# Optimization experiments

Measured on AMD Instinct MI355X. Metric: run time of the kernel, lower is better.

The kernel has to match this reference:

```python
import jax, jax.numpy as jnp
import numpy as np

EMBED_DIM = 1024
NUM_HEADS = 16
HEAD_DIM = EMBED_DIM // NUM_HEADS
B, S = 2, 2048


def setup_inputs() -> dict:
    key = jax.random.key(0)
    ks = jax.random.split(key, 11)
    scale = 1.0 / np.sqrt(EMBED_DIM)
    inp = {
        "q": jax.random.normal(ks[0], (B, S, EMBED_DIM), jnp.float32),
        "k": jax.random.normal(ks[1], (B, S, EMBED_DIM), jnp.float32),
        "v": jax.random.normal(ks[2], (B, S, EMBED_DIM), jnp.float32),
        "Wq": jax.random.normal(ks[3], (EMBED_DIM, EMBED_DIM), jnp.float32) * scale,
        "bq": jnp.zeros((EMBED_DIM,), jnp.float32),
        "Wk": jax.random.normal(ks[4], (EMBED_DIM, EMBED_DIM), jnp.float32) * scale,
        "bk": jnp.zeros((EMBED_DIM,), jnp.float32),
        "Wv": jax.random.normal(ks[5], (EMBED_DIM, EMBED_DIM), jnp.float32) * scale,
        "bv": jnp.zeros((EMBED_DIM,), jnp.float32),
        "Wo": jax.random.normal(ks[6], (EMBED_DIM, EMBED_DIM), jnp.float32) * scale,
        "bo": jnp.zeros((EMBED_DIM,), jnp.float32),
    }
    return inp


def _split_heads(x):
    # [B, S, E] -> [B, H, S, D]
    b, s, _ = x.shape
    return x.reshape(b, s, NUM_HEADS, HEAD_DIM).transpose(0, 2, 1, 3)


def reference(q, k, v, Wq, bq, Wk, bk, Wv, bv, Wo, bo):
    query = _split_heads(q @ Wq + bq)  # [B,H,S,D]
    key_ = _split_heads(k @ Wk + bk)
    value = _split_heads(v @ Wv + bv)
    # scaled dot-product attention (scale by sqrt(head_dim), as in source)
    logits = jnp.einsum("bhqd,bhkd->bhqk", query, key_) / jnp.sqrt(
        jnp.asarray(HEAD_DIM, jnp.float32)
    )
    weights = jax.nn.softmax(logits, axis=-1)
    attn = jnp.einsum("bhqk,bhkd->bhqd", weights, value)  # [B,H,S,D]
    concat = attn.transpose(0, 2, 1, 3).reshape(q.shape[0], -1, EMBED_DIM)
    return concat @ Wo + bo
```

## Files before the change

kernel.cpp:

```cpp
#include <hip/hip_runtime.h>
#include <hip/hip_bf16.h>
#include <math.h>


typedef short bf16x8 __attribute__((ext_vector_type(8)));
typedef short bf16x4 __attribute__((ext_vector_type(4)));
typedef float f32x4 __attribute__((ext_vector_type(4)));
typedef unsigned short u16;
typedef unsigned int u32;

#if defined(__HIP_DEVICE_COMPILE__) && __has_builtin(__builtin_amdgcn_mfma_f32_16x16x16_bf16)
#define MFMA16(a, b, c) __builtin_amdgcn_mfma_f32_16x16x16_bf16(a, b, c, 0, 0, 0)
#else
#define MFMA16(a, b, c) __builtin_amdgcn_mfma_f32_16x16x16bf16_1k(a, b, c, 0, 0, 0)
#endif

#define QSCALE 0.18033688011112042f

__device__ __forceinline__ u16 f2b(float f) {
  union { float f; unsigned u; } v; v.f = f;
  unsigned r = v.u + 0x7FFF + ((v.u >> 16) & 1);
  return (u16)(r >> 16);
}

__device__ __forceinline__ void glds16(const u16* g, u16* l) {
  __builtin_amdgcn_global_load_lds(
      (const __attribute__((address_space(1))) u32*)g,
      (__attribute__((address_space(3))) u32*)l, 16, 0, 0);
}

__global__ void cvt3_f32_bf16(const float* __restrict__ q, const float* __restrict__ k,
                              const float* __restrict__ v, u16* __restrict__ qo,
                              u16* __restrict__ ko, u16* __restrict__ vo) {
  const float* in = blockIdx.y == 0 ? q : (blockIdx.y == 1 ? k : v);
  u16* out = blockIdx.y == 0 ? qo : (blockIdx.y == 1 ? ko : vo);
  int i = (blockIdx.x * 256 + threadIdx.x) * 8;
  float4 a = *(const float4*)(in + i);
  float4 b = *(const float4*)(in + i + 4);
  union { u16 u[8]; uint4 v; } o;
  o.u[0] = f2b(a.x); o.u[1] = f2b(a.y); o.u[2] = f2b(a.z); o.u[3] = f2b(a.w);
  o.u[4] = f2b(b.x); o.u[5] = f2b(b.y); o.u[6] = f2b(b.z); o.u[7] = f2b(b.w);
  *(uint4*)(out + i) = o.v;
}

__global__ void transpose_w4(const float* __restrict__ W0, const float* __restrict__ W1,
                             const float* __restrict__ W2, const float* __restrict__ W3,
                             u16* __restrict__ T0, u16* __restrict__ T1,
                             u16* __restrict__ T2, u16* __restrict__ T3) {
  const float* W = blockIdx.z == 0 ? W0 : (blockIdx.z == 1 ? W1 : (blockIdx.z == 2 ? W2 : W3));
  u16* WT = blockIdx.z == 0 ? T0 : (blockIdx.z == 1 ? T1 : (blockIdx.z == 2 ? T2 : T3));
  __shared__ float tile[64][65];
  int k0 = blockIdx.y * 64, n0 = blockIdx.x * 64;
  int c = threadIdx.x & 63, r0 = threadIdx.x >> 6;
  #pragma unroll
  for (int i = 0; i < 64; i += 4)
    tile[r0 + i][c] = W[(k0 + r0 + i) * 1024 + n0 + c];
  __syncthreads();
  #pragma unroll
  for (int i = 0; i < 64; i += 4)
    WT[(n0 + r0 + i) * 1024 + k0 + c] = f2b(tile[c][r0 + i]);
}

template<int MODE>
__device__ __forceinline__ void gemm_core(
    const u16* __restrict__ A, const u16* __restrict__ BT,
    const float* __restrict__ bias, void* __restrict__ out,
    int bx, int by, float scale) {
  __shared__ u16 As[128 * 64];
  __shared__ u16 Bs[128 * 64];
  const int tid = threadIdx.x;
  const int w = tid >> 6, lane = tid & 63;
  const int wm = w >> 1, wn = w & 1;
  const int q = lane >> 4, l16 = lane & 15;
  const int m0 = by * 128, n0 = bx * 128;
  const int K = 1024;

  f32x4 acc[4][4] = {};
  for (int k0 = 0; k0 < K; k0 += 64) {
    __syncthreads();
    #pragma unroll
    for (int p = 0; p < 4; ++p) {
      int c = p * 4 + w;
      int ci = c * 64 + lane;
      int r = ci >> 3, b = ci & 7;
      glds16(A + (m0 + r) * K + k0 + ((b ^ (r & 7)) * 8), As + c * 512);
    }
    #pragma unroll
    for (int p = 0; p < 4; ++p) {
      int c = p * 4 + w;
      int ci = c * 64 + lane;
      int r = ci >> 3, b = ci & 7;
      glds16(BT + (n0 + r) * K + k0 + ((b ^ (r & 7)) * 8), Bs + c * 512);
    }
    __builtin_amdgcn_s_waitcnt(0xF70);
    __syncthreads();
    #pragma unroll
    for (int ks = 0; ks < 2; ++ks) {
      bf16x8 af[4], bf[4];
      #pragma unroll
      for (int mt = 0; mt < 4; ++mt) {
        int row = wm * 64 + mt * 16 + l16;
        af[mt] = *(const bf16x8*)(As + row * 64 + (((ks * 4 + q) ^ (row & 7)) * 8));
      }
      #pragma unroll
      for (int nt = 0; nt < 4; ++nt) {
        int row = wn * 64 + nt * 16 + l16;
        bf[nt] = *(const bf16x8*)(Bs + row * 64 + (((ks * 4 + q) ^ (row & 7)) * 8));
      }
      #pragma unroll
      for (int mt = 0; mt < 4; ++mt)
        #pragma unroll
        for (int nt = 0; nt < 4; ++nt)
          acc[mt][nt] = __builtin_amdgcn_mfma_f32_16x16x32_bf16(af[mt], bf[nt], acc[mt][nt], 0, 0, 0);
    }
  }
  #pragma unroll
  for (int mt = 0; mt < 4; ++mt)
    #pragma unroll
    for (int nt = 0; nt < 4; ++nt) {
      int col = n0 + wn * 64 + nt * 16 + l16;
      float bcol = bias[col];
      if (MODE == 2) {
        int rbase = m0 + wm * 64 + mt * 16 + q * 4;
        int b = rbase >> 11, s0 = rbase & 2047;
        int h = col >> 6, d = col & 63;
        union { u16 u[4]; uint2 v; } o;
        #pragma unroll
        for (int reg = 0; reg < 4; ++reg)
          o.u[reg] = f2b(acc[mt][nt][reg] + bcol);
        *(uint2*)((u16*)out + (((b << 4) + h) * 64 + d) * 2048 + s0) = o.v;
      } else {
        #pragma unroll
        for (int reg = 0; reg < 4; ++reg) {
          int row = m0 + wm * 64 + mt * 16 + q * 4 + reg;
          float val = (acc[mt][nt][reg] + bcol) * scale;
          if (MODE == 0) {
            int b = row >> 11, s = row & 2047, h = col >> 6, d = col & 63;
            ((u16*)out)[(((b << 4) + h) * 2048 + s) * 64 + d] = f2b(val);
          } else {
            ((float*)out)[row * 1024 + col] = val;
          }
        }
      }
    }
}

__global__ __launch_bounds__(256) void gemm_qkv(
    const u16* qb, const u16* kb, const u16* vb,
    const u16* WqT, const u16* WkT, const u16* WvT,
    const float* bq, const float* bk, const float* bv,
    u16* Qh, u16* Kh, u16* VhT) {
  int z = blockIdx.z;
  if (z == 0)      gemm_core<0>(qb, WqT, bq, Qh,  blockIdx.x, blockIdx.y, QSCALE);
  else if (z == 1) gemm_core<0>(kb, WkT, bk, Kh,  blockIdx.x, blockIdx.y, 1.0f);
  else             gemm_core<2>(vb, WvT, bv, VhT, blockIdx.x, blockIdx.y, 1.0f);
}

__global__ __launch_bounds__(256) void gemm_out(
    const u16* A, const u16* BT, const float* bias, float* out) {
  gemm_core<1>(A, BT, bias, out, blockIdx.x, blockIdx.y, 1.0f);
}

__global__ __launch_bounds__(256) void flash_attn(
    const u16* __restrict__ Qh, const u16* __restrict__ Kh,
    const u16* __restrict__ VTh, u16* __restrict__ Oo) {
  __shared__ u16 Ks[2][64 * 64];
  __shared__ u16 Vt[2][64 * 64];

  const int tid = threadIdx.x, w = tid >> 6, lane = tid & 63;
  const int q = lane >> 4, l16 = lane & 15;
  const int bh = blockIdx.x >> 4, qt = blockIdx.x & 15;
  const u16* Qp = Qh + (bh * 2048 + qt * 128) * 64;
  const u16* Kp = Kh + bh * 2048 * 64;
  const u16* Vp = VTh + bh * 64 * 2048;

  bf16x8 aq[2][2];
  #pragma unroll
  for (int rb = 0; rb < 2; ++rb)
    #pragma unroll
    for (int ks = 0; ks < 2; ++ks)
      aq[rb][ks] = *(const bf16x8*)(Qp + (w * 32 + rb * 16 + l16) * 64 + ks * 32 + q * 8);

  const int sr = (lane & 7) ^ (lane >> 3);
  auto stage = [&](int kt2, int buf) {
    #pragma unroll
    for (int p = 0; p < 2; ++p) {
      int c = p * 4 + w;
      int r = c * 8 + (lane >> 3);
      glds16(Kp + (kt2 * 64 + r) * 64 + sr * 8, &Ks[buf][c * 512]);
      glds16(Vp + r * 2048 + kt2 * 64 + sr * 8, &Vt[buf][c * 512]);
    }
  };
  stage(0, 0);

  f32x4 oacc[4][2] = {};
  float lacc[2] = {0.f, 0.f};

  for (int kt = 0; kt < 32; ++kt) {
    const int cur = kt & 1;
    __builtin_amdgcn_s_waitcnt(0xF70);
    __syncthreads();
    if (kt + 1 < 32) stage(kt + 1, cur ^ 1);

    f32x4 st[2][4] = {};
    #pragma unroll
    for (int ks = 0; ks < 2; ++ks) {
      bf16x8 bk[4];
      #pragma unroll
      for (int nt = 0; nt < 4; ++nt) {
        int row = nt * 16 + l16;
        bk[nt] = *(const bf16x8*)(&Ks[cur][row * 64 + (((ks * 4 + q) ^ (l16 & 7)) * 8)]);
      }
      #pragma unroll
      for (int rb = 0; rb < 2; ++rb)
        #pragma unroll
        for (int nt = 0; nt < 4; ++nt)
          st[rb][nt] = __builtin_amdgcn_mfma_f32_16x16x32_bf16(bk[nt], aq[rb][ks], st[rb][nt], 0, 0, 0);
    }

    #pragma unroll
    for (int rb = 0; rb < 2; ++rb)
      #pragma unroll
      for (int nt = 0; nt < 4; ++nt)
        #pragma unroll
        for (int reg = 0; reg < 4; ++reg) {
          float p = __builtin_amdgcn_exp2f(st[rb][nt][reg]);
          lacc[rb] += p;
          st[rb][nt][reg] = p;
        }

    #pragma unroll
    for (int kb = 0; kb < 4; ++kb) {
      bf16x4 pf[2];
      #pragma unroll
      for (int rb = 0; rb < 2; ++rb) {
        union { u32 u[2]; bf16x4 v; } pk;
        pk.u[0] = __builtin_amdgcn_perm(__float_as_uint(st[rb][kb][1]),
                                        __float_as_uint(st[rb][kb][0]), 0x07060302u);
        pk.u[1] = __builtin_amdgcn_perm(__float_as_uint(st[rb][kb][3]),
                                        __float_as_uint(st[rb][kb][2]), 0x07060302u);
        pf[rb] = pk.v;
      }
      #pragma unroll
      for (int ntd = 0; ntd < 4; ++ntd) {
        int row = ntd * 16 + l16;
        int c = kb * 2 + (q >> 1);
        bf16x4 vf = *(const bf16x4*)(&Vt[cur][row * 64 + ((c ^ (l16 & 7)) * 8) + (q & 1) * 4]);
        #pragma unroll
        for (int rb = 0; rb < 2; ++rb)
          oacc[ntd][rb] = MFMA16(vf, pf[rb], oacc[ntd][rb]);
      }
    }
  }

  float rl[2];
  #pragma unroll
  for (int rb = 0; rb < 2; ++rb) {
    float s = lacc[rb];
    s += __shfl_xor(s, 16);
    s += __shfl_xor(s, 32);
    rl[rb] = 0.998046875f / s;
  }

  const int b = bh >> 4, h = bh & 15;
  #pragma unroll
  for (int rb = 0; rb < 2; ++rb) {
    int row = b * 2048 + qt * 128 + w * 32 + rb * 16 + l16;
    #pragma unroll
    for (int ntd = 0; ntd < 4; ++ntd) {
      union { u16 u[4]; uint2 v; } o;
      #pragma unroll
      for (int reg = 0; reg < 4; ++reg)
        o.u[reg] = f2b(oacc[ntd][rb][reg] * rl[rb]);
      *(uint2*)(Oo + row * 1024 + h * 64 + ntd * 16 + q * 4) = o.v;
    }
  }
}

extern "C" void kernel_launch(void* const* d_in, const int* in_sizes, int n_in,
                              void* d_out, int out_size, void* d_ws, size_t ws_size,
                              hipStream_t stream) {
  const float* q  = (const float*)d_in[0];
  const float* k  = (const float*)d_in[1];
  const float* v  = (const float*)d_in[2];
  const float* Wq = (const float*)d_in[3];
  const float* bq = (const float*)d_in[4];
  const float* Wk = (const float*)d_in[5];
  const float* bk = (const float*)d_in[6];
  const float* Wv = (const float*)d_in[7];
  const float* bv = (const float*)d_in[8];
  const float* Wo = (const float*)d_in[9];
  const float* bo = (const float*)d_in[10];

  char* ws = (char*)d_ws;
  const size_t MB = 1024 * 1024;
  u16* qb  = (u16*)(ws);
  u16* kb  = (u16*)(ws + 8 * MB);
  u16* vb  = (u16*)(ws + 16 * MB);
  u16* WqT = (u16*)(ws + 24 * MB);
  u16* WkT = (u16*)(ws + 26 * MB);
  u16* WvT = (u16*)(ws + 28 * MB);
  u16* WoT = (u16*)(ws + 30 * MB);
  u16* Qh  = (u16*)(ws + 32 * MB);
  u16* Kh  = (u16*)(ws + 40 * MB);
  u16* VhT = (u16*)(ws + 48 * MB);
  u16* Ao  = (u16*)(ws + 56 * MB);

  cvt3_f32_bf16<<<dim3(2048, 3), 256, 0, stream>>>(q, k, v, qb, kb, vb);
  transpose_w4<<<dim3(16, 16, 4), 256, 0, stream>>>(Wq, Wk, Wv, Wo, WqT, WkT, WvT, WoT);
  gemm_qkv<<<dim3(8, 32, 3), 256, 0, stream>>>(qb, kb, vb, WqT, WkT, WvT,
                                               bq, bk, bv, Qh, Kh, VhT);
  flash_attn<<<512, 256, 0, stream>>>(Qh, Kh, VhT, Ao);
  gemm_out<<<dim3(8, 32), 256, 0, stream>>>(Ao, WoT, bo, (float*)d_out);
}
```

Measured before the change: 245.1 us.

## Use narrower output GEMM tiles and stage two KV tiles per attention barrier

The output projection GEMM is templated on tile width and now runs with 128x64 tiles, doubling its grid from 256 to 512 blocks so more CUs on the device have work. Flash attention now loads two 64-key tiles per stage, which halves the number of barriers and waits per head. Its block index mapping is reordered so consecutive blocks cover different heads. The attention kernel's shared memory doubles, which may reduce occupancy.

```diff
diff --git a/kernel.cpp b/kernel.cpp
--- a/kernel.cpp
+++ b/kernel.cpp
@@ -61,21 +61,22 @@
     WT[(n0 + r0 + i) * 1024 + k0 + c] = f2b(tile[c][r0 + i]);
 }
 
-template<int MODE>
+template<int MODE, int BN>
 __device__ __forceinline__ void gemm_core(
     const u16* __restrict__ A, const u16* __restrict__ BT,
     const float* __restrict__ bias, void* __restrict__ out,
     int bx, int by, float scale) {
+  constexpr int NT = BN / 64 * 2;
   __shared__ u16 As[128 * 64];
-  __shared__ u16 Bs[128 * 64];
+  __shared__ u16 Bs[BN * 64];
   const int tid = threadIdx.x;
   const int w = tid >> 6, lane = tid & 63;
   const int wm = w >> 1, wn = w & 1;
   const int q = lane >> 4, l16 = lane & 15;
-  const int m0 = by * 128, n0 = bx * 128;
+  const int m0 = by * 128, n0 = bx * BN;
   const int K = 1024;
 
-  f32x4 acc[4][4] = {};
+  f32x4 acc[4][NT] = {};
   for (int k0 = 0; k0 < K; k0 += 64) {
     __syncthreads();
     #pragma unroll
@@ -86,7 +87,7 @@
       glds16(A + (m0 + r) * K + k0 + ((b ^ (r & 7)) * 8), As + c * 512);
     }
     #pragma unroll
-    for (int p = 0; p < 4; ++p) {
+    for (int p = 0; p < BN / 32; ++p) {
       int c = p * 4 + w;
       int ci = c * 64 + lane;
       int r = ci >> 3, b = ci & 7;
@@ -96,29 +97,29 @@
     __syncthreads();
     #pragma unroll
     for (int ks = 0; ks < 2; ++ks) {
-      bf16x8 af[4], bf[4];
+      bf16x8 af[4], bf[NT];
       #pragma unroll
       for (int mt = 0; mt < 4; ++mt) {
         int row = wm * 64 + mt * 16 + l16;
         af[mt] = *(const bf16x8*)(As + row * 64 + (((ks * 4 + q) ^ (row & 7)) * 8));
       }
       #pragma unroll
-      for (int nt = 0; nt < 4; ++nt) {
-        int row = wn * 64 + nt * 16 + l16;
+      for (int nt = 0; nt < NT; ++nt) {
+        int row = wn * (BN / 2) + nt * 16 + l16;
         bf[nt] = *(const bf16x8*)(Bs + row * 64 + (((ks * 4 + q) ^ (row & 7)) * 8));
       }
       #pragma unroll
       for (int mt = 0; mt < 4; ++mt)
         #pragma unroll
-        for (int nt = 0; nt < 4; ++nt)
+        for (int nt = 0; nt < NT; ++nt)
           acc[mt][nt] = __builtin_amdgcn_mfma_f32_16x16x32_bf16(af[mt], bf[nt], acc[mt][nt], 0, 0, 0);
     }
   }
   #pragma unroll
   for (int mt = 0; mt < 4; ++mt)
     #pragma unroll
-    for (int nt = 0; nt < 4; ++nt) {
-      int col = n0 + wn * 64 + nt * 16 + l16;
+    for (int nt = 0; nt < NT; ++nt) {
+      int col = n0 + wn * (BN / 2) + nt * 16 + l16;
       float bcol = bias[col];
       if (MODE == 2) {
         int rbase = m0 + wm * 64 + mt * 16 + q * 4;
@@ -151,25 +152,25 @@
     const float* bq, const float* bk, const float* bv,
     u16* Qh, u16* Kh, u16* VhT) {
   int z = blockIdx.z;
-  if (z == 0)      gemm_core<0>(qb, WqT, bq, Qh,  blockIdx.x, blockIdx.y, QSCALE);
-  else if (z == 1) gemm_core<0>(kb, WkT, bk, Kh,  blockIdx.x, blockIdx.y, 1.0f);
-  else             gemm_core<2>(vb, WvT, bv, VhT, blockIdx.x, blockIdx.y, 1.0f);
+  if (z == 0)      gemm_core<0, 128>(qb, WqT, bq, Qh,  blockIdx.x, blockIdx.y, QSCALE);
+  else if (z == 1) gemm_core<0, 128>(kb, WkT, bk, Kh,  blockIdx.x, blockIdx.y, 1.0f);
+  else             gemm_core<2, 128>(vb, WvT, bv, VhT, blockIdx.x, blockIdx.y, 1.0f);
 }
 
 __global__ __launch_bounds__(256) void gemm_out(
     const u16* A, const u16* BT, const float* bias, float* out) {
-  gemm_core<1>(A, BT, bias, out, blockIdx.x, blockIdx.y, 1.0f);
+  gemm_core<1, 64>(A, BT, bias, out, blockIdx.x, blockIdx.y, 1.0f);
 }
 
 __global__ __launch_bounds__(256) void flash_attn(
     const u16* __restrict__ Qh, const u16* __restrict__ Kh,
     const u16* __restrict__ VTh, u16* __restrict__ Oo) {
-  __shared__ u16 Ks[2][64 * 64];
-  __shared__ u16 Vt[2][64 * 64];
+  __shared__ u16 Ks[2][8192];
+  __shared__ u16 Vt[2][8192];
 
   const int tid = threadIdx.x, w = tid >> 6, lane = tid & 63;
   const int q = lane >> 4, l16 = lane & 15;
-  const int bh = blockIdx.x >> 4, qt = blockIdx.x & 15;
+  const int bh = blockIdx.x & 31, qt = blockIdx.x >> 5;
   const u16* Qp = Qh + (bh * 2048 + qt * 128) * 64;
   const u16* Kp = Kh + bh * 2048 * 64;
   const u16* Vp = VTh + bh * 64 * 2048;
@@ -184,11 +185,16 @@
   const int sr = (lane & 7) ^ (lane >> 3);
   auto stage = [&](int kt2, int buf) {
     #pragma unroll
-    for (int p = 0; p < 2; ++p) {
+    for (int p = 0; p < 4; ++p) {
       int c = p * 4 + w;
       int r = c * 8 + (lane >> 3);
       glds16(Kp + (kt2 * 64 + r) * 64 + sr * 8, &Ks[buf][c * 512]);
-      glds16(Vp + r * 2048 + kt2 * 64 + sr * 8, &Vt[buf][c * 512]);
+    }
+    #pragma unroll
+    for (int p = 0; p < 4; ++p) {
+      int c = p * 4 + w;
+      int r = (c & 7) * 8 + (lane >> 3);
+      glds16(Vp + r * 2048 + (kt2 + (c >> 3)) * 64 + sr * 8, &Vt[buf][c * 512]);
     }
   };
   stage(0, 0);
@@ -196,59 +202,65 @@
   f32x4 oacc[4][2] = {};
   float lacc[2] = {0.f, 0.f};
 
-  for (int kt = 0; kt < 32; ++kt) {
-    const int cur = kt & 1;
+  for (int kt = 0; kt < 32; kt += 2) {
+    const int buf = (kt >> 1) & 1;
     __builtin_amdgcn_s_waitcnt(0xF70);
     __syncthreads();
-    if (kt + 1 < 32) stage(kt + 1, cur ^ 1);
-
-    f32x4 st[2][4] = {};
-    #pragma unroll
-    for (int ks = 0; ks < 2; ++ks) {
-      bf16x8 bk[4];
-      #pragma unroll
-      for (int nt = 0; nt < 4; ++nt) {
-        int row = nt * 16 + l16;
-        bk[nt] = *(const bf16x8*)(&Ks[cur][row * 64 + (((ks * 4 + q) ^ (l16 & 7)) * 8)]);
-      }
+    if (kt + 2 < 32) stage(kt + 2, buf ^ 1);
+
+    #pragma unroll
+    for (int t = 0; t < 2; ++t) {
+      const u16* KsT = &Ks[buf][t * 4096];
+      const u16* VtT = &Vt[buf][t * 4096];
+
+      f32x4 st[2][4] = {};
+      #pragma unroll
+      for (int ks = 0; ks < 2; ++ks) {
+        bf16x8 bk[4];
+        #pragma unroll
+        for (int nt = 0; nt < 4; ++nt) {
+          int row = nt * 16 + l16;
+          bk[nt] = *(const bf16x8*)(KsT + row * 64 + (((ks * 4 + q) ^ (l16 & 7)) * 8));
+        }
+        #pragma unroll
+        for (int rb = 0; rb < 2; ++rb)
+          #pragma unroll
+          for (int nt = 0; nt < 4; ++nt)
+            st[rb][nt] = __builtin_amdgcn_mfma_f32_16x16x32_bf16(bk[nt], aq[rb][ks], st[rb][nt], 0, 0, 0);
+      }
+
       #pragma unroll
       for (int rb = 0; rb < 2; ++rb)
         #pragma unroll
         for (int nt = 0; nt < 4; ++nt)
-          st[rb][nt] = __builtin_amdgcn_mfma_f32_16x16x32_bf16(bk[nt], aq[rb][ks], st[rb][nt], 0, 0, 0);
-    }
-
-    #pragma unroll
-    for (int rb = 0; rb < 2; ++rb)
-      #pragma unroll
-      for (int nt = 0; nt < 4; ++nt)
-        #pragma unroll
-        for (int reg = 0; reg < 4; ++reg) {
-          float p = __builtin_amdgcn_exp2f(st[rb][nt][reg]);
-          lacc[rb] += p;
-          st[rb][nt][reg] = p;
+          #pragma unroll
+          for (int reg = 0; reg < 4; ++reg) {
+            float p = __builtin_amdgcn_exp2f(st[rb][nt][reg]);
+            lacc[rb] += p;
+            st[rb][nt][reg] = p;
+          }
+
+      #pragma unroll
+      for (int kb = 0; kb < 4; ++kb) {
+        bf16x4 pf[2];
+        #pragma unroll
+        for (int rb = 0; rb < 2; ++rb) {
+          union { u32 u[2]; bf16x4 v; } pk;
+          pk.u[0] = __builtin_amdgcn_perm(__float_as_uint(st[rb][kb][1]),
+                                          __float_as_uint(st[rb][kb][0]), 0x07060302u);
+          pk.u[1] = __builtin_amdgcn_perm(__float_as_uint(st[rb][kb][3]),
+                                          __float_as_uint(st[rb][kb][2]), 0x07060302u);
+          pf[rb] = pk.v;
         }
-
-    #pragma unroll
-    for (int kb = 0; kb < 4; ++kb) {
-      bf16x4 pf[2];
-      #pragma unroll
-      for (int rb = 0; rb < 2; ++rb) {
-        union { u32 u[2]; bf16x4 v; } pk;
-        pk.u[0] = __builtin_amdgcn_perm(__float_as_uint(st[rb][kb][1]),
-                                        __float_as_uint(st[rb][kb][0]), 0x07060302u);
-        pk.u[1] = __builtin_amdgcn_perm(__float_as_uint(st[rb][kb][3]),
-                                        __float_as_uint(st[rb][kb][2]), 0x07060302u);
-        pf[rb] = pk.v;
-      }
-      #pragma unroll
-      for (int ntd = 0; ntd < 4; ++ntd) {
-        int row = ntd * 16 + l16;
-        int c = kb * 2 + (q >> 1);
-        bf16x4 vf = *(const bf16x4*)(&Vt[cur][row * 64 + ((c ^ (l16 & 7)) * 8) + (q & 1) * 4]);
-        #pragma unroll
-        for (int rb = 0; rb < 2; ++rb)
-          oacc[ntd][rb] = MFMA16(vf, pf[rb], oacc[ntd][rb]);
+        #pragma unroll
+        for (int ntd = 0; ntd < 4; ++ntd) {
+          int row = ntd * 16 + l16;
+          int c = kb * 2 + (q >> 1);
+          bf16x4 vf = *(const bf16x4*)(VtT + row * 64 + ((c ^ (l16 & 7)) * 8) + (q & 1) * 4);
+          #pragma unroll
+          for (int rb = 0; rb < 2; ++rb)
+            oacc[ntd][rb] = MFMA16(vf, pf[rb], oacc[ntd][rb]);
+        }
       }
     }
   }
@@ -311,5 +323,5 @@
   gemm_qkv<<<dim3(8, 32, 3), 256, 0, stream>>>(qb, kb, vb, WqT, WkT, WvT,
                                                bq, bk, bv, Qh, Kh, VhT);
   flash_attn<<<512, 256, 0, stream>>>(Qh, Kh, VhT, Ao);
-  gemm_out<<<dim3(8, 32), 256, 0, stream>>>(Ao, WoT, bo, (float*)d_out);
-}
+  gemm_out<<<dim3(16, 32), 256, 0, stream>>>(Ao, WoT, bo, (float*)d_out);
+}
```

New measurement: 229.5 us. 6.4% less time.
